# Kernel optimization log

Measured on AMD Instinct MI355X. Metric: run time of the kernel, lower is better.

Reference implementation:

```python
import jax, jax.numpy as jnp
import numpy as np

ATTN_WINDOW = 128
HIDDEN = 1024
NUM_HEADS = 16


def _sliding_window_attention(q, k, v, w):
    # q,k,v: [B, H, S, D]; each query i attends to keys j with |i-j| <= w.
    B, nh, S, D = q.shape
    nc = S // w  # number of query chunks of size w
    # pad keys/values by w on each side so chunk c sees padded positions [c*w, c*w+3w)
    k_pad = jnp.pad(k, ((0, 0), (0, 0), (w, w), (0, 0)))
    v_pad = jnp.pad(v, ((0, 0), (0, 0), (w, w), (0, 0)))
    idx = (jnp.arange(nc) * w)[:, None] + jnp.arange(3 * w)[None, :]  # [nc, 3w]
    k_c = k_pad[:, :, idx, :]  # [B, H, nc, 3w, D]
    v_c = v_pad[:, :, idx, :]  # [B, H, nc, 3w, D]
    q_c = q.reshape(B, nh, nc, w, D)
    # banded scores: [B, H, nc, w, 3w] (no 1/sqrt(d) scaling in original)
    scores = jnp.einsum('bhcid,bhcjd->bhcij', q_c, k_c)
    i = jnp.arange(w)[:, None]            # query offset in chunk
    j = jnp.arange(3 * w)[None, :]        # key offset in padded 3w block
    band = jnp.abs((j - w) - i) <= w      # [w, 3w] within-window mask
    key_pos = (jnp.arange(nc) * w)[:, None, None] + j[None, :, :] - w  # [nc, 1, 3w]
    valid = band[None, :, :] & (key_pos >= 0) & (key_pos < S)  # [nc, w, 3w]
    big_neg = jnp.finfo(scores.dtype).min
    scores = jnp.where(valid[None, None], scores, big_neg)
    probs = jax.nn.softmax(scores, axis=-1)
    out = jnp.einsum('bhcij,bhcjd->bhcid', probs, v_c)  # [B, H, nc, w, D]
    return out.reshape(B, nh, S, D)


def setup_inputs() -> dict:
    key = jax.random.key(0)
    k1, k2, k3 = jax.random.split(key, 3)
    B, S = 2, 8192
    query = jax.random.normal(k1, (B, S, HIDDEN), dtype=jnp.float32)
    key_t = jax.random.normal(k2, (B, S, HIDDEN), dtype=jnp.float32)
    value = jax.random.normal(k3, (B, S, HIDDEN), dtype=jnp.float32)
    return {"query": query, "key": key_t, "value": value}


def reference(query, key, value):
    B, S, _ = query.shape
    D = HIDDEN // NUM_HEADS
    q = query.reshape(B, S, NUM_HEADS, D).transpose(0, 2, 1, 3)
    k = key.reshape(B, S, NUM_HEADS, D).transpose(0, 2, 1, 3)
    v = value.reshape(B, S, NUM_HEADS, D).transpose(0, 2, 1, 3)
    out = _sliding_window_attention(q, k, v, ATTN_WINDOW)  # [B, H, S, D]
    return out.transpose(0, 2, 1, 3).reshape(B, S, HIDDEN)
```

## Files before the change

kernel.cpp:

```cpp
#include <hip/hip_runtime.h>

#define S_LEN 8192
#define HID   1024
#define NHEAD 16
#define DH    64
#define WIN   128
#define NCHUNK (S_LEN / WIN)
#define NC2    (NCHUNK / 2)

typedef _Float16 half8   __attribute__((ext_vector_type(8)));
typedef _Float16 half4_t __attribute__((ext_vector_type(4)));
typedef float    f32x4   __attribute__((ext_vector_type(4)));

#define QPITCH 72
#define PPITCH 132

__global__ __launch_bounds__(512, 2)
void swa_fwd(const float* __restrict__ qg,
             const float* __restrict__ kg,
             const float* __restrict__ vg,
             float* __restrict__ og)
{
    const int c    = blockIdx.x;
    const int h    = blockIdx.y;
    const int b    = blockIdx.z;
    const int tid  = threadIdx.x;
    const int wave = tid >> 6;
    const int lane = tid & 63;
    const int l16  = lane & 15;
    const int quad = lane >> 4;
    const int hs   = wave >> 2;

    __shared__ _Float16 sK [128 * QPITCH];
    __shared__ _Float16 sVt[ 64 * PPITCH];

    const size_t qbase  = (((size_t)b * S_LEN + (size_t)c * (2 * WIN)) * HID) + (size_t)h * DH;
    const size_t kvbase = (((size_t)b * S_LEN) * HID) + (size_t)h * DH;

    half8 qf[2][2];
    #pragma unroll
    for (int mt = 0; mt < 2; ++mt) {
        const int row = wave * 32 + mt * 16 + l16;
        const float* qrow = qg + qbase + (size_t)row * HID;
        #pragma unroll
        for (int kk = 0; kk < 2; ++kk) {
            const float4 a = *(const float4*)(qrow + kk * 32 + quad * 8);
            const float4 d = *(const float4*)(qrow + kk * 32 + quad * 8 + 4);
            qf[mt][kk] = (half8){ (_Float16)a.x, (_Float16)a.y, (_Float16)a.z, (_Float16)a.w,
                                  (_Float16)d.x, (_Float16)d.y, (_Float16)d.z, (_Float16)d.w };
        }
    }

    f32x4 Oacc[2][4];
    #pragma unroll
    for (int mt = 0; mt < 2; ++mt)
        #pragma unroll
        for (int dt = 0; dt < 4; ++dt) Oacc[mt][dt] = (f32x4){0.f, 0.f, 0.f, 0.f};
    float m_i[2] = { -3.0e38f, -3.0e38f };
    float l_i[2] = { 0.0f, 0.0f };

    const int t0 = (c == 0)       ? 1 : 0;
    const int t1 = (c == NC2 - 1) ? 2 : 3;
    const float L2E = 1.44269504088896f;

    const int r0 = tid >> 4;
    const int c4 = (tid & 15) * 4;
    float4 kreg[4], vreg[4];

    auto loadtile = [&](int t) {
        const size_t kb = kvbase + (size_t)(c * (2 * WIN) + (t - 1) * WIN) * HID;
        #pragma unroll
        for (int p = 0; p < 4; ++p) {
            const int row = p * 32 + r0;
            kreg[p] = *(const float4*)(kg + kb + (size_t)row * HID + c4);
            vreg[p] = *(const float4*)(vg + kb + (size_t)row * HID + c4);
        }
    };

    loadtile(t0);

    for (int t = t0; t <= t1; ++t) {
        __syncthreads();
        #pragma unroll
        for (int p = 0; p < 4; ++p) {
            const int row = p * 32 + r0;
            const float4 f = kreg[p];
            half4_t hk = { (_Float16)f.x, (_Float16)f.y, (_Float16)f.z, (_Float16)f.w };
            *(half4_t*)&sK[row * QPITCH + c4] = hk;
            const float4 g = vreg[p];
            sVt[(c4 + 0) * PPITCH + row] = (_Float16)g.x;
            sVt[(c4 + 1) * PPITCH + row] = (_Float16)g.y;
            sVt[(c4 + 2) * PPITCH + row] = (_Float16)g.z;
            sVt[(c4 + 3) * PPITCH + row] = (_Float16)g.w;
        }
        __syncthreads();

        if (t < t1) loadtile(t + 1);

        const int role = t - hs;
        if (role >= 0 && role <= 2) {
            #pragma unroll
            for (int mt = 0; mt < 2; ++mt) {
                f32x4 Sacc[8];
                #pragma unroll
                for (int nt = 0; nt < 8; ++nt) Sacc[nt] = (f32x4){0.f, 0.f, 0.f, 0.f};
                __builtin_amdgcn_s_setprio(1);
                #pragma unroll
                for (int kk = 0; kk < 2; ++kk) {
                    #pragma unroll
                    for (int nt = 0; nt < 8; ++nt) {
                        const half8 kf = *(const half8*)&sK[(nt * 16 + l16) * QPITCH + kk * 32 + quad * 8];
                        Sacc[nt] = __builtin_amdgcn_mfma_f32_16x16x32_f16(kf, qf[mt][kk], Sacc[nt], 0, 0, 0);
                    }
                }
                __builtin_amdgcn_s_setprio(0);

                const int iq = (wave & 3) * 32 + mt * 16 + l16;
                if (role != 1) {
                    #pragma unroll
                    for (int nt = 0; nt < 8; ++nt) {
                        #pragma unroll
                        for (int r = 0; r < 4; ++r) {
                            const int j = nt * 16 + quad * 4 + r;
                            const bool valid = (role == 0) ? (j >= iq) : (j <= iq);
                            if (!valid) Sacc[nt][r] = -3.0e38f;
                        }
                    }
                }

                float mx = fmaxf(fmaxf(Sacc[0][0], Sacc[0][1]), fmaxf(Sacc[0][2], Sacc[0][3]));
                #pragma unroll
                for (int nt = 1; nt < 8; ++nt)
                    mx = fmaxf(mx, fmaxf(fmaxf(Sacc[nt][0], Sacc[nt][1]),
                                         fmaxf(Sacc[nt][2], Sacc[nt][3])));
                mx = fmaxf(mx, __shfl_xor(mx, 16, 64));
                mx = fmaxf(mx, __shfl_xor(mx, 32, 64));
                const float mnew = fmaxf(m_i[mt], mx);
                const float alpha = exp2f((m_i[mt] - mnew) * L2E);
                m_i[mt] = mnew;

                #pragma unroll
                for (int dt = 0; dt < 4; ++dt) {
                    Oacc[mt][dt][0] *= alpha; Oacc[mt][dt][1] *= alpha;
                    Oacc[mt][dt][2] *= alpha; Oacc[mt][dt][3] *= alpha;
                }

                float rs = 0.0f;
                __builtin_amdgcn_s_setprio(1);
                #pragma unroll
                for (int nt = 0; nt < 8; ++nt) {
                    const float p0 = exp2f((Sacc[nt][0] - mnew) * L2E);
                    const float p1 = exp2f((Sacc[nt][1] - mnew) * L2E);
                    const float p2 = exp2f((Sacc[nt][2] - mnew) * L2E);
                    const float p3 = exp2f((Sacc[nt][3] - mnew) * L2E);
                    rs += (p0 + p1) + (p2 + p3);
                    const auto plo = __builtin_amdgcn_cvt_pkrtz(p0, p1);
                    const auto phi = __builtin_amdgcn_cvt_pkrtz(p2, p3);
                    const half4_t pf = (half4_t){ (_Float16)plo.x, (_Float16)plo.y,
                                                  (_Float16)phi.x, (_Float16)phi.y };
                    #pragma unroll
                    for (int dt = 0; dt < 4; ++dt) {
                        const half4_t vf = *(const half4_t*)&sVt[(dt * 16 + l16) * PPITCH + nt * 16 + quad * 4];
                        Oacc[mt][dt] = __builtin_amdgcn_mfma_f32_16x16x16f16(vf, pf, Oacc[mt][dt], 0, 0, 0);
                    }
                }
                __builtin_amdgcn_s_setprio(0);

                rs += __shfl_xor(rs, 16, 64);
                rs += __shfl_xor(rs, 32, 64);
                l_i[mt] = l_i[mt] * alpha + rs;
            }
        }
    }

    #pragma unroll
    for (int mt = 0; mt < 2; ++mt) {
        const float inv = 1.0f / l_i[mt];
        const int row = wave * 32 + mt * 16 + l16;
        float* orow = og + qbase + (size_t)row * HID;
        #pragma unroll
        for (int dt = 0; dt < 4; ++dt) {
            float4 o = { Oacc[mt][dt][0] * inv, Oacc[mt][dt][1] * inv,
                         Oacc[mt][dt][2] * inv, Oacc[mt][dt][3] * inv };
            *(float4*)(orow + dt * 16 + quad * 4) = o;
        }
    }
}

extern "C" void kernel_launch(void* const* d_in, const int* in_sizes, int n_in,
                              void* d_out, int out_size, void* d_ws, size_t ws_size,
                              hipStream_t stream) {
    const float* q = (const float*)d_in[0];
    const float* k = (const float*)d_in[1];
    const float* v = (const float*)d_in[2];
    float* out = (float*)d_out;
    dim3 grid(NC2, NHEAD, 2);
    dim3 block(512);
    swa_fwd<<<grid, block, 0, stream>>>(q, k, v, out);
}
```

Measured before the change: 272.5 us.

## Skip fully-masked key tiles in band edges and balance query tiles across waves

```diff
diff --git a/kernel.cpp b/kernel.cpp
--- a/kernel.cpp
+++ b/kernel.cpp
@@ -30,6 +30,7 @@
     const int l16  = lane & 15;
     const int quad = lane >> 4;
     const int hs   = wave >> 2;
+    const int w    = wave & 3;
 
     __shared__ _Float16 sK [128 * QPITCH];
     __shared__ _Float16 sVt[ 64 * PPITCH];
@@ -40,7 +41,8 @@
     half8 qf[2][2];
     #pragma unroll
     for (int mt = 0; mt < 2; ++mt) {
-        const int row = wave * 32 + mt * 16 + l16;
+        const int tidx = (mt == 0) ? w : (7 - w);
+        const int row  = hs * 128 + tidx * 16 + l16;
         const float* qrow = qg + qbase + (size_t)row * HID;
         #pragma unroll
         for (int kk = 0; kk < 2; ++kk) {
@@ -101,38 +103,40 @@
         if (role >= 0 && role <= 2) {
             #pragma unroll
             for (int mt = 0; mt < 2; ++mt) {
+                const int tidx = (mt == 0) ? w : (7 - w);
+                const int lo   = (role == 0) ? tidx : 0;
+                const int hi   = (role == 2) ? tidx : 7;
+
                 f32x4 Sacc[8];
-                #pragma unroll
-                for (int nt = 0; nt < 8; ++nt) Sacc[nt] = (f32x4){0.f, 0.f, 0.f, 0.f};
                 __builtin_amdgcn_s_setprio(1);
                 #pragma unroll
-                for (int kk = 0; kk < 2; ++kk) {
+                for (int nt = 0; nt < 8; ++nt) {
+                    if (nt < lo || nt > hi) continue;
+                    f32x4 acc = (f32x4){0.f, 0.f, 0.f, 0.f};
                     #pragma unroll
-                    for (int nt = 0; nt < 8; ++nt) {
+                    for (int kk = 0; kk < 2; ++kk) {
                         const half8 kf = *(const half8*)&sK[(nt * 16 + l16) * QPITCH + kk * 32 + quad * 8];
-                        Sacc[nt] = __builtin_amdgcn_mfma_f32_16x16x32_f16(kf, qf[mt][kk], Sacc[nt], 0, 0, 0);
+                        acc = __builtin_amdgcn_mfma_f32_16x16x32_f16(kf, qf[mt][kk], acc, 0, 0, 0);
                     }
-                }
-                __builtin_amdgcn_s_setprio(0);
-
-                const int iq = (wave & 3) * 32 + mt * 16 + l16;
-                if (role != 1) {
-                    #pragma unroll
-                    for (int nt = 0; nt < 8; ++nt) {
+                    if (role != 1 && nt == tidx) {
                         #pragma unroll
                         for (int r = 0; r < 4; ++r) {
-                            const int j = nt * 16 + quad * 4 + r;
-                            const bool valid = (role == 0) ? (j >= iq) : (j <= iq);
-                            if (!valid) Sacc[nt][r] = -3.0e38f;
+                            const int jj = quad * 4 + r;
+                            const bool valid = (role == 0) ? (jj >= l16) : (jj <= l16);
+                            if (!valid) acc[r] = -3.0e38f;
                         }
                     }
-                }
-
-                float mx = fmaxf(fmaxf(Sacc[0][0], Sacc[0][1]), fmaxf(Sacc[0][2], Sacc[0][3]));
-                #pragma unroll
-                for (int nt = 1; nt < 8; ++nt)
+                    Sacc[nt] = acc;
+                }
+                __builtin_amdgcn_s_setprio(0);
+
+                float mx = -3.0e38f;
+                #pragma unroll
+                for (int nt = 0; nt < 8; ++nt) {
+                    if (nt < lo || nt > hi) continue;
                     mx = fmaxf(mx, fmaxf(fmaxf(Sacc[nt][0], Sacc[nt][1]),
                                          fmaxf(Sacc[nt][2], Sacc[nt][3])));
+                }
                 mx = fmaxf(mx, __shfl_xor(mx, 16, 64));
                 mx = fmaxf(mx, __shfl_xor(mx, 32, 64));
                 const float mnew = fmaxf(m_i[mt], mx);
@@ -149,6 +153,7 @@
                 __builtin_amdgcn_s_setprio(1);
                 #pragma unroll
                 for (int nt = 0; nt < 8; ++nt) {
+                    if (nt < lo || nt > hi) continue;
                     const float p0 = exp2f((Sacc[nt][0] - mnew) * L2E);
                     const float p1 = exp2f((Sacc[nt][1] - mnew) * L2E);
                     const float p2 = exp2f((Sacc[nt][2] - mnew) * L2E);
@@ -176,7 +181,8 @@
     #pragma unroll
     for (int mt = 0; mt < 2; ++mt) {
         const float inv = 1.0f / l_i[mt];
-        const int row = wave * 32 + mt * 16 + l16;
+        const int tidx = (mt == 0) ? w : (7 - w);
+        const int row  = hs * 128 + tidx * 16 + l16;
         float* orow = og + qbase + (size_t)row * HID;
         #pragma unroll
         for (int dt = 0; dt < 4; ++dt) {
```

Measured after the change: 269.2 us. Within noise of the previous version (-1.2%).
